# Performance work log

Hardware: AMD Instinct MI355X
Metric: run time of the kernel (lower is better)

The kernel has to match this reference:

```python
import math
import jax, jax.numpy as jnp
import numpy as np

B, S, HID = 1, 2048, 4096
NH, NKV, D = 32, 8, 128
THETA = 10000.0


def setup_inputs() -> dict:
    key = jax.random.key(0)
    k1, k2, k3, k4, k5 = jax.random.split(key, 5)
    hidden_states = jax.random.normal(k1, (B, S, HID), dtype=jnp.float32)
    k_cache = jax.random.normal(k2, (B, NKV, S, D), dtype=jnp.float32)
    v_cache = jax.random.normal(k3, (B, NKV, S, D), dtype=jnp.float32)
    Wq = jax.random.normal(k4, (HID, NH * D), dtype=jnp.float32) * 0.02
    Wo = jax.random.normal(k5, (NH * D, HID), dtype=jnp.float32) * 0.02
    position_ids = jnp.broadcast_to(jnp.arange(S, dtype=jnp.int32), (B, S))
    # causal mask: True = masked out (torch.where(mask, -10000, scores))
    attention_mask = jnp.broadcast_to(
        jnp.triu(jnp.ones((S, S), dtype=bool), k=1)[None, None], (B, 1, S, S)
    )
    return {
        "hidden_states": hidden_states,
        "k_cache": k_cache,
        "v_cache": v_cache,
        "Wq": Wq,
        "Wo": Wo,
        "position_ids": position_ids,
        "attention_mask": attention_mask,
    }


def _rotate_half(x):
    x1, x2 = jnp.split(x, 2, axis=-1)
    return jnp.concatenate([-x2, x1], axis=-1)


def _rope_tables(position_ids):
    # Llama rotary embedding gathered at position_ids -> [B, 1, S, D]
    inv_freq = 1.0 / (THETA ** (jnp.arange(0, D, 2, dtype=jnp.float32) / D))
    freqs = position_ids[..., None].astype(jnp.float32) * inv_freq  # [B, S, D/2]
    emb = jnp.concatenate([freqs, freqs], axis=-1)  # [B, S, D]
    return jnp.cos(emb)[:, None], jnp.sin(emb)[:, None]


def reference(hidden_states, k_cache, v_cache, Wq, Wo, position_ids, attention_mask):
    G = NH // NKV  # GQA group size
    # q projection: [B, S, HID] -> [B, NH, S, D]
    q = (hidden_states @ Wq).reshape(B, S, NH, D).transpose(0, 2, 1, 3)
    cos, sin = _rope_tables(position_ids)
    q = q * cos + _rotate_half(q) * sin
    # GQA without materializing repeat_kv: group query heads over kv heads
    qg = q.reshape(B, NKV, G, S, D)
    scores = jnp.einsum("bkgsd,bktd->bkgst", qg, k_cache) / math.sqrt(D)
    scores = scores.reshape(B, NH, S, S)
    scores = jnp.where(attention_mask, jnp.float32(-10000.0), scores)
    probs = jax.nn.softmax(scores.astype(jnp.float32), axis=-1).astype(q.dtype)
    out = jnp.einsum("bkgst,bktd->bkgsd", probs.reshape(B, NKV, G, S, S), v_cache)
    out = out.reshape(B, NH, S, D).transpose(0, 2, 1, 3).reshape(B, S, NH * D)
    return out @ Wo
```

## Files before the change

### kernel.cpp

```cpp
#include <hip/hip_runtime.h>
#include <cstdint>
#include <cstddef>

#define S_LEN 2048
#define HID 4096
#define NH 32
#define NKV 8
#define HD 128

typedef __attribute__((ext_vector_type(4))) float f32x4;
typedef __attribute__((ext_vector_type(8))) short bf16x8;

__device__ __forceinline__ unsigned short f2bf(float f) {
  union { float f; uint32_t u; } v; v.f = f;
  uint32_t r = v.u + 0x7FFFu + ((v.u >> 16) & 1u);
  return (unsigned short)(r >> 16);
}

__global__ void cvt_bf16_kernel(const float* __restrict__ in,
                                unsigned short* __restrict__ out, int n4) {
  int i = blockIdx.x * blockDim.x + threadIdx.x;
  if (i >= n4) return;
  float4 v = ((const float4*)in)[i];
  ushort4 o;
  o.x = f2bf(v.x); o.y = f2bf(v.y); o.z = f2bf(v.z); o.w = f2bf(v.w);
  ((ushort4*)out)[i] = o;
}

__global__ __launch_bounds__(256) void transpose_cvt2_kernel(
    const float* __restrict__ in0, unsigned short* __restrict__ out0,
    const float* __restrict__ in1, unsigned short* __restrict__ out1,
    int R, int C) {
  __shared__ float tile[64][65];
  const float* inb = (blockIdx.z == 0) ? in0 : in1;
  unsigned short* outb = (blockIdx.z == 0) ? out0 : out1;
  const int c0 = blockIdx.x * 64, r0 = blockIdx.y * 64;
  const int tid = threadIdx.x;
#pragma unroll
  for (int p = 0; p < 4; ++p) {
    const int ch = p * 256 + tid;
    const int r = ch >> 4, off = (ch & 15) << 2;
    *(float4*)&tile[r][off] = *(const float4*)(inb + (size_t)(r0 + r) * C + c0 + off);
  }
  __syncthreads();
#pragma unroll
  for (int p = 0; p < 2; ++p) {
    const int ch = p * 256 + tid;
    const int i = ch >> 3, j0 = (ch & 7) << 3;
    bf16x8 v;
#pragma unroll
    for (int k = 0; k < 8; ++k) v[k] = (short)f2bf(tile[j0 + k][i]);
    *(bf16x8*)(outb + (size_t)(c0 + i) * R + r0 + j0) = v;
  }
}

__global__ __launch_bounds__(256) void transpose_cvt_kernel(
    const float* __restrict__ in, unsigned short* __restrict__ out, int R, int C) {
  __shared__ float tile[64][65];
  const int b = blockIdx.z;
  const float* inb = in + (size_t)b * R * C;
  unsigned short* outb = out + (size_t)b * R * C;
  const int c0 = blockIdx.x * 64, r0 = blockIdx.y * 64;
  const int tid = threadIdx.x;
#pragma unroll
  for (int p = 0; p < 4; ++p) {
    const int ch = p * 256 + tid;
    const int r = ch >> 4, off = (ch & 15) << 2;
    *(float4*)&tile[r][off] = *(const float4*)(inb + (size_t)(r0 + r) * C + c0 + off);
  }
  __syncthreads();
#pragma unroll
  for (int p = 0; p < 2; ++p) {
    const int ch = p * 256 + tid;
    const int i = ch >> 3, j0 = (ch & 7) << 3;
    bf16x8 v;
#pragma unroll
    for (int k = 0; k < 8; ++k) v[k] = (short)f2bf(tile[j0 + k][i]);
    *(bf16x8*)(outb + (size_t)(c0 + i) * R + r0 + j0) = v;
  }
}

__global__ __launch_bounds__(256, 2) void gemm_bt_kernel(
    const unsigned short* __restrict__ A, const unsigned short* __restrict__ BT,
    float* __restrict__ C, int M, int N, int K) {
  __shared__ __align__(16) unsigned short As[128 * 64];
  __shared__ __align__(16) unsigned short Bs[128 * 64];
  const int tid = threadIdx.x;
  const int lane = tid & 63;
  const int wid = tid >> 6;
  const int wm = (wid >> 1) * 64, wn = (wid & 1) * 64;
  const int g = blockIdx.x;
  const int xcd = g & 7, local = g >> 3;
  const int m0 = (xcd * 2 + (local & 1)) * 128;
  const int n0 = (local >> 1) * 128;
  const int lr = lane & 15;
  const int quad = lane >> 4;
  const int sw = lr & 7;
  f32x4 acc[4][4] = {};
  for (int kt = 0; kt < K; kt += 64) {
    __syncthreads();
#pragma unroll
    for (int p = 0; p < 4; ++p) {
      const int c = p * 256 + tid;
      const int r = c >> 3, jsrc = (c & 7) ^ (r & 7);
      __builtin_amdgcn_global_load_lds(
          (const __attribute__((address_space(1))) void*)(A + (size_t)(m0 + r) * K + kt + jsrc * 8),
          (__attribute__((address_space(3))) void*)(As + c * 8), 16, 0, 0);
      __builtin_amdgcn_global_load_lds(
          (const __attribute__((address_space(1))) void*)(BT + (size_t)(n0 + r) * K + kt + jsrc * 8),
          (__attribute__((address_space(3))) void*)(Bs + c * 8), 16, 0, 0);
    }
    __syncthreads();
#pragma unroll
    for (int h = 0; h < 2; ++h) {
      const int pos = ((h * 4 + quad) ^ sw) << 3;
      bf16x8 a[4], b[4];
#pragma unroll
      for (int t = 0; t < 4; ++t) {
        a[t] = *(const bf16x8*)(As + (wm + t * 16 + lr) * 64 + pos);
        b[t] = *(const bf16x8*)(Bs + (wn + t * 16 + lr) * 64 + pos);
      }
#pragma unroll
      for (int mt = 0; mt < 4; ++mt)
#pragma unroll
        for (int nt = 0; nt < 4; ++nt)
          acc[mt][nt] = __builtin_amdgcn_mfma_f32_16x16x32_bf16(a[mt], b[nt], acc[mt][nt], 0, 0, 0);
    }
  }
  const int qd = quad << 2;
#pragma unroll
  for (int mt = 0; mt < 4; ++mt)
#pragma unroll
    for (int nt = 0; nt < 4; ++nt) {
      const int row = m0 + wm + mt * 16 + qd;
      const int col = n0 + wn + nt * 16 + lr;
#pragma unroll
      for (int r = 0; r < 4; ++r)
        C[(size_t)(row + r) * N + col] = acc[mt][nt][r];
    }
}

__global__ __launch_bounds__(256, 2) void gemm_rope_kernel(
    const unsigned short* __restrict__ A, const unsigned short* __restrict__ BT,
    const int* __restrict__ pos_ids, unsigned short* __restrict__ Qout) {
  __shared__ __align__(16) unsigned short As[128 * 64];
  __shared__ __align__(16) unsigned short Bs[128 * 64];
  const int tid = threadIdx.x;
  const int lane = tid & 63;
  const int wid = tid >> 6;
  const int wm = wid * 32;
  const int g = blockIdx.x;
  const int xcd = g & 7, local = g >> 3;
  const int m0 = (xcd * 2 + (local & 1)) * 128;
  const int n0 = (local >> 1) * 128;
  const int lr = lane & 15;
  const int quad = lane >> 4;
  const int sw = lr & 7;
  f32x4 acc[2][8] = {};
  for (int kt = 0; kt < HID; kt += 64) {
    __syncthreads();
#pragma unroll
    for (int p = 0; p < 4; ++p) {
      const int c = p * 256 + tid;
      const int r = c >> 3, jsrc = (c & 7) ^ (r & 7);
      __builtin_amdgcn_global_load_lds(
          (const __attribute__((address_space(1))) void*)(A + (size_t)(m0 + r) * HID + kt + jsrc * 8),
          (__attribute__((address_space(3))) void*)(As + c * 8), 16, 0, 0);
      __builtin_amdgcn_global_load_lds(
          (const __attribute__((address_space(1))) void*)(BT + (size_t)(n0 + r) * HID + kt + jsrc * 8),
          (__attribute__((address_space(3))) void*)(Bs + c * 8), 16, 0, 0);
    }
    __syncthreads();
#pragma unroll
    for (int h = 0; h < 2; ++h) {
      const int pos = ((h * 4 + quad) ^ sw) << 3;
      bf16x8 a[2], b[8];
#pragma unroll
      for (int t = 0; t < 2; ++t)
        a[t] = *(const bf16x8*)(As + (wm + t * 16 + lr) * 64 + pos);
#pragma unroll
      for (int t = 0; t < 8; ++t)
        b[t] = *(const bf16x8*)(Bs + (t * 16 + lr) * 64 + pos);
#pragma unroll
      for (int mt = 0; mt < 2; ++mt)
#pragma unroll
        for (int nt = 0; nt < 8; ++nt)
          acc[mt][nt] = __builtin_amdgcn_mfma_f32_16x16x32_bf16(a[mt], b[nt], acc[mt][nt], 0, 0, 0);
    }
  }
  const int qd = quad << 2;
  const int h = n0 >> 7;
#pragma unroll
  for (int mt = 0; mt < 2; ++mt)
#pragma unroll
    for (int r = 0; r < 4; ++r) {
      const int row = m0 + wm + mt * 16 + qd + r;
      const float pos = (float)pos_ids[row];
#pragma unroll
      for (int nt = 0; nt < 4; ++nt) {
        const int i = nt * 16 + lr;
        const float invf = __expf(-(float)(2 * i) * (9.2103403719761836f / 128.0f));
        float sn, cs;
        __sincosf(pos * invf, &sn, &cs);
        const float x1 = acc[mt][nt][r], x2 = acc[mt][nt + 4][r];
        Qout[((size_t)h * S_LEN + row) * HD + i]      = f2bf(x1 * cs - x2 * sn);
        Qout[((size_t)h * S_LEN + row) * HD + i + 64] = f2bf(x2 * cs + x1 * sn);
      }
    }
}

__global__ __launch_bounds__(256, 2) void attn_kernel(
    const unsigned short* __restrict__ Q, const unsigned short* __restrict__ Kc,
    const unsigned short* __restrict__ VT, unsigned short* __restrict__ Aout) {
  __shared__ __align__(16) unsigned short Ks[64 * 136];
  __shared__ __align__(16) unsigned short Vs[128 * 72];
  __shared__ __align__(16) unsigned short Ps[128 * 72];
  const int tid = threadIdx.x, lane = tid & 63, wid = tid >> 6;
  const int qh = blockIdx.x;
  const int qt = (blockIdx.y < 8) ? (15 - (int)blockIdx.y) : ((int)blockIdx.y - 8);
  const int kvh = qh >> 2;
  const int lr = lane & 15, quad = lane >> 4;
  const float scale = 0.08838834764831843f;

  bf16x8 qf[2][4];
#pragma unroll
  for (int mt = 0; mt < 2; ++mt)
#pragma unroll
    for (int kk = 0; kk < 4; ++kk)
      qf[mt][kk] = *(const bf16x8*)(Q + ((size_t)qh * S_LEN + qt * 128 + wid * 32 + mt * 16 + lr) * HD + kk * 32 + quad * 8);

  f32x4 o[2][8] = {};
  float lsum[2] = {0.f, 0.f};

  const int prow0 = (wid * 32 + lr) * 72;
  const int nkt = 2 * qt + 2;
  for (int kt2 = 0; kt2 < nkt; ++kt2) {
    bf16x8 kr[4], vr[4];
#pragma unroll
    for (int p = 0; p < 4; ++p) {
      const int c = p * 256 + tid;
      kr[p] = *(const bf16x8*)(Kc + ((size_t)kvh * S_LEN + kt2 * 64 + (c >> 4)) * HD + (c & 15) * 8);
      vr[p] = *(const bf16x8*)(VT + ((size_t)kvh * HD + (c >> 3)) * S_LEN + kt2 * 64 + (c & 7) * 8);
    }
    __syncthreads();
#pragma unroll
    for (int p = 0; p < 4; ++p) {
      const int c = p * 256 + tid;
      *(bf16x8*)(Ks + (c >> 4) * 136 + (c & 15) * 8) = kr[p];
      *(bf16x8*)(Vs + (c >> 3) * 72 + (c & 7) * 8) = vr[p];
    }
    __syncthreads();

    const bool dtile = (kt2 >= 2 * qt);
#pragma unroll
    for (int nt = 0; nt < 4; ++nt) {
      f32x4 s0 = {}, s1 = {};
#pragma unroll
      for (int kk = 0; kk < 4; ++kk) {
        bf16x8 kf = *(const bf16x8*)(Ks + (nt * 16 + lr) * 136 + kk * 32 + quad * 8);
        s0 = __builtin_amdgcn_mfma_f32_16x16x32_bf16(kf, qf[0][kk], s0, 0, 0, 0);
        s1 = __builtin_amdgcn_mfma_f32_16x16x32_bf16(kf, qf[1][kk], s1, 0, 0, 0);
      }
      const int skey0 = kt2 * 64 + nt * 16 + quad * 4;
#pragma unroll
      for (int mt = 0; mt < 2; ++mt) {
        const f32x4 s = mt ? s1 : s0;
        const int qrow = qt * 128 + wid * 32 + mt * 16 + lr;
        ushort4 pk;
        float ls = 0.f;
        float pv[4];
#pragma unroll
        for (int r = 0; r < 4; ++r) {
          float v = s[r] * scale - 16.0f;
          if (dtile && (skey0 + r) > qrow) v = -1e30f;
          pv[r] = __expf(v);
          ls += pv[r];
        }
        pk.x = f2bf(pv[0]); pk.y = f2bf(pv[1]); pk.z = f2bf(pv[2]); pk.w = f2bf(pv[3]);
        lsum[mt] += ls;
        *(ushort4*)(Ps + prow0 + mt * 16 * 72 + nt * 16 + quad * 4) = pk;
      }
    }
    bf16x8 pf[2][2];
#pragma unroll
    for (int mt = 0; mt < 2; ++mt)
#pragma unroll
      for (int kk = 0; kk < 2; ++kk)
        pf[mt][kk] = *(const bf16x8*)(Ps + prow0 + mt * 16 * 72 + kk * 32 + quad * 8);
#pragma unroll
    for (int dt = 0; dt < 8; ++dt)
#pragma unroll
      for (int kk = 0; kk < 2; ++kk) {
        bf16x8 vf = *(const bf16x8*)(Vs + (dt * 16 + lr) * 72 + kk * 32 + quad * 8);
        o[0][dt] = __builtin_amdgcn_mfma_f32_16x16x32_bf16(vf, pf[0][kk], o[0][dt], 0, 0, 0);
        o[1][dt] = __builtin_amdgcn_mfma_f32_16x16x32_bf16(vf, pf[1][kk], o[1][dt], 0, 0, 0);
      }
  }

#pragma unroll
  for (int mt = 0; mt < 2; ++mt) {
    float l = lsum[mt];
    l += __shfl_xor(l, 16);
    l += __shfl_xor(l, 32);
    const float inv = 1.0f / l;
    const int qrow = qt * 128 + wid * 32 + mt * 16 + lr;
#pragma unroll
    for (int dt = 0; dt < 8; ++dt) {
      ushort4 w;
      w.x = f2bf(o[mt][dt][0] * inv);
      w.y = f2bf(o[mt][dt][1] * inv);
      w.z = f2bf(o[mt][dt][2] * inv);
      w.w = f2bf(o[mt][dt][3] * inv);
      *(ushort4*)(Aout + (size_t)qrow * HID + qh * HD + dt * 16 + quad * 4) = w;
    }
  }
}

extern "C" void kernel_launch(void* const* d_in, const int* in_sizes, int n_in,
                              void* d_out, int out_size, void* d_ws, size_t ws_size,
                              hipStream_t stream) {
  const float* hidden  = (const float*)d_in[0];
  const float* k_cache = (const float*)d_in[1];
  const float* v_cache = (const float*)d_in[2];
  const float* Wq      = (const float*)d_in[3];
  const float* Wo      = (const float*)d_in[4];
  const int*   pos     = (const int*)d_in[5];
  float* out = (float*)d_out;

  char* ws = (char*)d_ws;
  unsigned short* hidden_bf = (unsigned short*)(ws + 0);
  unsigned short* attn_bf   = hidden_bf;
  unsigned short* WqT       = (unsigned short*)(ws + 16777216);
  unsigned short* WoT       = (unsigned short*)(ws + 50331648);
  unsigned short* k_bf      = (unsigned short*)(ws + 83886080);
  unsigned short* vT        = (unsigned short*)(ws + 88080384);
  unsigned short* q_bf      = (unsigned short*)(ws + 92274688);

  cvt_bf16_kernel<<<(S_LEN * HID / 4 + 255) / 256, 256, 0, stream>>>(hidden, hidden_bf, S_LEN * HID / 4);
  cvt_bf16_kernel<<<(NKV * S_LEN * HD / 4 + 255) / 256, 256, 0, stream>>>(k_cache, k_bf, NKV * S_LEN * HD / 4);
  transpose_cvt2_kernel<<<dim3(HID / 64, HID / 64, 2), 256, 0, stream>>>(Wq, WqT, Wo, WoT, HID, HID);
  transpose_cvt_kernel<<<dim3(HD / 64, S_LEN / 64, NKV), 256, 0, stream>>>(v_cache, vT, S_LEN, HD);

  gemm_rope_kernel<<<dim3((S_LEN / 128) * (HID / 128)), 256, 0, stream>>>(hidden_bf, WqT, pos, q_bf);
  attn_kernel<<<dim3(NH, S_LEN / 128), 256, 0, stream>>>(q_bf, k_bf, vT, attn_bf);
  gemm_bt_kernel<<<dim3((S_LEN / 128) * (HID / 128)), 256, 0, stream>>>(attn_bf, WoT, out, S_LEN, HID, HID);
}
```

Baseline: 421.4 us.

## Double-buffer attention K/V via direct global-to-LDS loads with swizzle and register P

Rewrites the attention inner loop to double-buffer K and V tiles in LDS using global_load_lds, with an XOR swizzle replacing padding to avoid bank conflicts. The probability tile no longer round-trips through shared memory; it is rearranged in registers with permlane swaps. exp2 with a folded scale, packed bf16 conversion instructions and s_setprio around MFMA blocks are also added. Together these aim to overlap loads with compute and cut LDS traffic and ALU work. The cost is more complex lane-permutation logic and reliance on gfx950-specific instructions, which could be wrong if the lane mapping is off.

```diff
diff --git a/kernel.cpp b/kernel.cpp
--- a/kernel.cpp
+++ b/kernel.cpp
@@ -15,6 +15,20 @@
   union { float f; uint32_t u; } v; v.f = f;
   uint32_t r = v.u + 0x7FFFu + ((v.u >> 16) & 1u);
   return (unsigned short)(r >> 16);
+}
+
+__device__ __forceinline__ float exp2_fast(float x) {
+#if __has_builtin(__builtin_amdgcn_exp2f)
+  return __builtin_amdgcn_exp2f(x);
+#else
+  float r; asm("v_exp_f32 %0, %1" : "=v"(r) : "v"(x)); return r;
+#endif
+}
+
+__device__ __forceinline__ unsigned int cvt_pk_bf16(float lo, float hi) {
+  unsigned int r;
+  asm("v_cvt_pk_bf16_f32 %0, %1, %2" : "=v"(r) : "v"(lo), "v"(hi));
+  return r;
 }
 
 __global__ void cvt_bf16_kernel(const float* __restrict__ in,
@@ -212,15 +226,15 @@
 __global__ __launch_bounds__(256, 2) void attn_kernel(
     const unsigned short* __restrict__ Q, const unsigned short* __restrict__ Kc,
     const unsigned short* __restrict__ VT, unsigned short* __restrict__ Aout) {
-  __shared__ __align__(16) unsigned short Ks[64 * 136];
-  __shared__ __align__(16) unsigned short Vs[128 * 72];
-  __shared__ __align__(16) unsigned short Ps[128 * 72];
+  __shared__ __align__(16) unsigned short Ks[2][64 * 128];
+  __shared__ __align__(16) unsigned short Vs[2][128 * 64];
   const int tid = threadIdx.x, lane = tid & 63, wid = tid >> 6;
   const int qh = blockIdx.x;
   const int qt = (blockIdx.y < 8) ? (15 - (int)blockIdx.y) : ((int)blockIdx.y - 8);
   const int kvh = qh >> 2;
   const int lr = lane & 15, quad = lane >> 4;
-  const float scale = 0.08838834764831843f;
+  const float SC = 0.12751619754705767f;
+  const float NB = -23.083120654223414f;
 
   bf16x8 qf[2][4];
 #pragma unroll
@@ -231,70 +245,101 @@
 
   f32x4 o[2][8] = {};
   float lsum[2] = {0.f, 0.f};
-
-  const int prow0 = (wid * 32 + lr) * 72;
   const int nkt = 2 * qt + 2;
-  for (int kt2 = 0; kt2 < nkt; ++kt2) {
-    bf16x8 kr[4], vr[4];
+  const int swz = lr & 7;
+
+  auto stage = [&](int buf, int kt2) {
 #pragma unroll
     for (int p = 0; p < 4; ++p) {
       const int c = p * 256 + tid;
-      kr[p] = *(const bf16x8*)(Kc + ((size_t)kvh * S_LEN + kt2 * 64 + (c >> 4)) * HD + (c & 15) * 8);
-      vr[p] = *(const bf16x8*)(VT + ((size_t)kvh * HD + (c >> 3)) * S_LEN + kt2 * 64 + (c & 7) * 8);
-    }
-    __syncthreads();
-#pragma unroll
-    for (int p = 0; p < 4; ++p) {
-      const int c = p * 256 + tid;
-      *(bf16x8*)(Ks + (c >> 4) * 136 + (c & 15) * 8) = kr[p];
-      *(bf16x8*)(Vs + (c >> 3) * 72 + (c & 7) * 8) = vr[p];
-    }
-    __syncthreads();
-
+      const int kr = c >> 4, kj = (c & 15) ^ (kr & 7);
+      __builtin_amdgcn_global_load_lds(
+          (const __attribute__((address_space(1))) void*)(Kc + ((size_t)kvh * S_LEN + kt2 * 64 + kr) * HD + kj * 8),
+          (__attribute__((address_space(3))) void*)(&Ks[buf][c * 8]), 16, 0, 0);
+      const int vr = c >> 3, vj = (c & 7) ^ (vr & 7);
+      __builtin_amdgcn_global_load_lds(
+          (const __attribute__((address_space(1))) void*)(VT + ((size_t)kvh * HD + vr) * S_LEN + kt2 * 64 + vj * 8),
+          (__attribute__((address_space(3))) void*)(&Vs[buf][c * 8]), 16, 0, 0);
+    }
+  };
+
+  stage(0, 0);
+  __syncthreads();
+
+  for (int kt2 = 0; kt2 < nkt; ++kt2) {
+    const int cur = kt2 & 1;
+    if (kt2 + 1 < nkt) stage(cur ^ 1, kt2 + 1);
+    const unsigned short* KsC = Ks[cur];
+    const unsigned short* VsC = Vs[cur];
     const bool dtile = (kt2 >= 2 * qt);
+
+    uint32_t Pw[2][4][2];
 #pragma unroll
     for (int nt = 0; nt < 4; ++nt) {
       f32x4 s0 = {}, s1 = {};
+      __builtin_amdgcn_s_setprio(1);
 #pragma unroll
       for (int kk = 0; kk < 4; ++kk) {
-        bf16x8 kf = *(const bf16x8*)(Ks + (nt * 16 + lr) * 136 + kk * 32 + quad * 8);
+        bf16x8 kf = *(const bf16x8*)(KsC + (nt * 16 + lr) * 128 + (((kk * 4 + quad) ^ swz) * 8));
         s0 = __builtin_amdgcn_mfma_f32_16x16x32_bf16(kf, qf[0][kk], s0, 0, 0, 0);
         s1 = __builtin_amdgcn_mfma_f32_16x16x32_bf16(kf, qf[1][kk], s1, 0, 0, 0);
       }
+      __builtin_amdgcn_s_setprio(0);
       const int skey0 = kt2 * 64 + nt * 16 + quad * 4;
 #pragma unroll
       for (int mt = 0; mt < 2; ++mt) {
         const f32x4 s = mt ? s1 : s0;
         const int qrow = qt * 128 + wid * 32 + mt * 16 + lr;
-        ushort4 pk;
+        float pv[4];
         float ls = 0.f;
-        float pv[4];
 #pragma unroll
         for (int r = 0; r < 4; ++r) {
-          float v = s[r] * scale - 16.0f;
+          float v = fmaf(s[r], SC, NB);
           if (dtile && (skey0 + r) > qrow) v = -1e30f;
-          pv[r] = __expf(v);
+          pv[r] = exp2_fast(v);
           ls += pv[r];
         }
-        pk.x = f2bf(pv[0]); pk.y = f2bf(pv[1]); pk.z = f2bf(pv[2]); pk.w = f2bf(pv[3]);
         lsum[mt] += ls;
-        *(ushort4*)(Ps + prow0 + mt * 16 * 72 + nt * 16 + quad * 4) = pk;
-      }
-    }
+        Pw[mt][nt][0] = cvt_pk_bf16(pv[0], pv[1]);
+        Pw[mt][nt][1] = cvt_pk_bf16(pv[2], pv[3]);
+      }
+    }
+
     bf16x8 pf[2][2];
 #pragma unroll
     for (int mt = 0; mt < 2; ++mt)
 #pragma unroll
-      for (int kk = 0; kk < 2; ++kk)
-        pf[mt][kk] = *(const bf16x8*)(Ps + prow0 + mt * 16 * 72 + kk * 32 + quad * 8);
+      for (int k = 0; k < 2; ++k) {
+        uint32_t w4[4];
+#pragma unroll
+        for (int w = 0; w < 2; ++w) {
+          uint32_t x = Pw[mt][2 * k][w], y = Pw[mt][2 * k + 1][w];
+          asm("v_permlane32_swap_b32 %0, %1" : "+v"(x), "+v"(y));
+          uint32_t xe = x, xo = x;
+          asm("v_permlane16_swap_b32 %0, %1" : "+v"(xe), "+v"(xo));
+          uint32_t ye = y, yo = y;
+          asm("v_permlane16_swap_b32 %0, %1" : "+v"(ye), "+v"(yo));
+          const bool qodd = (quad & 1) != 0;
+          w4[0 + w] = qodd ? ye : xe;
+          w4[2 + w] = qodd ? yo : xo;
+        }
+        union { uint32_t u[4]; bf16x8 v; } P;
+        P.u[0] = w4[0]; P.u[1] = w4[1]; P.u[2] = w4[2]; P.u[3] = w4[3];
+        pf[mt][k] = P.v;
+      }
+
+    __builtin_amdgcn_s_setprio(1);
 #pragma unroll
     for (int dt = 0; dt < 8; ++dt)
 #pragma unroll
       for (int kk = 0; kk < 2; ++kk) {
-        bf16x8 vf = *(const bf16x8*)(Vs + (dt * 16 + lr) * 72 + kk * 32 + quad * 8);
+        bf16x8 vf = *(const bf16x8*)(VsC + (dt * 16 + lr) * 64 + (((kk * 4 + quad) ^ swz) * 8));
         o[0][dt] = __builtin_amdgcn_mfma_f32_16x16x32_bf16(vf, pf[0][kk], o[0][dt], 0, 0, 0);
         o[1][dt] = __builtin_amdgcn_mfma_f32_16x16x32_bf16(vf, pf[1][kk], o[1][dt], 0, 0, 0);
       }
+    __builtin_amdgcn_s_setprio(0);
+
+    __syncthreads();
   }
 
 #pragma unroll
@@ -306,12 +351,10 @@
     const int qrow = qt * 128 + wid * 32 + mt * 16 + lr;
 #pragma unroll
     for (int dt = 0; dt < 8; ++dt) {
-      ushort4 w;
-      w.x = f2bf(o[mt][dt][0] * inv);
-      w.y = f2bf(o[mt][dt][1] * inv);
-      w.z = f2bf(o[mt][dt][2] * inv);
-      w.w = f2bf(o[mt][dt][3] * inv);
-      *(ushort4*)(Aout + (size_t)qrow * HID + qh * HD + dt * 16 + quad * 4) = w;
+      uint2 w;
+      w.x = cvt_pk_bf16(o[mt][dt][0] * inv, o[mt][dt][1] * inv);
+      w.y = cvt_pk_bf16(o[mt][dt][2] * inv, o[mt][dt][3] * inv);
+      *(uint2*)(Aout + (size_t)qrow * HID + qh * HD + dt * 16 + quad * 4) = w;
     }
   }
 }
```

Result: no change. 427.6 us (+1.5%).

## Double-buffer GEMM LDS tiles and use exp2/packed bf16 converts in attention

Applied to the files above, without the earlier changes.

Both projection GEMMs now stage the next K-tile into a second LDS buffer with global_load_lds while the current tile feeds the MFMAs. This leaves one barrier per iteration instead of two and is meant to hide global load latency. The attention softmax folds scale and offset into one FMA with log2e pre-multiplied and calls the hardware exp2. It also packs bf16 with v_cvt_pk_bf16_f32 in place of the software rounding routine. Doubling LDS to 64KB per block may limit occupancy under launch_bounds(256,2), and the async LDS writes rely on the trailing barrier for correctness.

```diff
diff --git a/kernel.cpp b/kernel.cpp
--- a/kernel.cpp
+++ b/kernel.cpp
@@ -15,6 +15,20 @@
   union { float f; uint32_t u; } v; v.f = f;
   uint32_t r = v.u + 0x7FFFu + ((v.u >> 16) & 1u);
   return (unsigned short)(r >> 16);
+}
+
+__device__ __forceinline__ float exp2_fast(float x) {
+#if __has_builtin(__builtin_amdgcn_exp2f)
+  return __builtin_amdgcn_exp2f(x);
+#else
+  float r; asm("v_exp_f32 %0, %1" : "=v"(r) : "v"(x)); return r;
+#endif
+}
+
+__device__ __forceinline__ unsigned int cvt_pk_bf16(float lo, float hi) {
+  unsigned int r;
+  asm("v_cvt_pk_bf16_f32 %0, %1, %2" : "=v"(r) : "v"(lo), "v"(hi));
+  return r;
 }
 
 __global__ void cvt_bf16_kernel(const float* __restrict__ in,
@@ -83,8 +97,8 @@
 __global__ __launch_bounds__(256, 2) void gemm_bt_kernel(
     const unsigned short* __restrict__ A, const unsigned short* __restrict__ BT,
     float* __restrict__ C, int M, int N, int K) {
-  __shared__ __align__(16) unsigned short As[128 * 64];
-  __shared__ __align__(16) unsigned short Bs[128 * 64];
+  __shared__ __align__(16) unsigned short As[2][128 * 64];
+  __shared__ __align__(16) unsigned short Bs[2][128 * 64];
   const int tid = threadIdx.x;
   const int lane = tid & 63;
   const int wid = tid >> 6;
@@ -96,29 +110,38 @@
   const int lr = lane & 15;
   const int quad = lane >> 4;
   const int sw = lr & 7;
-  f32x4 acc[4][4] = {};
-  for (int kt = 0; kt < K; kt += 64) {
-    __syncthreads();
+  const int nkt = K >> 6;
+
+  auto stage = [&](int buf, int kt) {
 #pragma unroll
     for (int p = 0; p < 4; ++p) {
       const int c = p * 256 + tid;
       const int r = c >> 3, jsrc = (c & 7) ^ (r & 7);
       __builtin_amdgcn_global_load_lds(
-          (const __attribute__((address_space(1))) void*)(A + (size_t)(m0 + r) * K + kt + jsrc * 8),
-          (__attribute__((address_space(3))) void*)(As + c * 8), 16, 0, 0);
+          (const __attribute__((address_space(1))) void*)(A + (size_t)(m0 + r) * K + kt * 64 + jsrc * 8),
+          (__attribute__((address_space(3))) void*)(&As[buf][c * 8]), 16, 0, 0);
       __builtin_amdgcn_global_load_lds(
-          (const __attribute__((address_space(1))) void*)(BT + (size_t)(n0 + r) * K + kt + jsrc * 8),
-          (__attribute__((address_space(3))) void*)(Bs + c * 8), 16, 0, 0);
-    }
-    __syncthreads();
+          (const __attribute__((address_space(1))) void*)(BT + (size_t)(n0 + r) * K + kt * 64 + jsrc * 8),
+          (__attribute__((address_space(3))) void*)(&Bs[buf][c * 8]), 16, 0, 0);
+    }
+  };
+
+  f32x4 acc[4][4] = {};
+  stage(0, 0);
+  __syncthreads();
+  int bufv = 0;
+  for (int t = 0; t < nkt; ++t) {
+    if (t + 1 < nkt) stage(bufv ^ 1, t + 1);
+    const unsigned short* as = As[bufv];
+    const unsigned short* bs = Bs[bufv];
 #pragma unroll
     for (int h = 0; h < 2; ++h) {
       const int pos = ((h * 4 + quad) ^ sw) << 3;
       bf16x8 a[4], b[4];
 #pragma unroll
-      for (int t = 0; t < 4; ++t) {
-        a[t] = *(const bf16x8*)(As + (wm + t * 16 + lr) * 64 + pos);
-        b[t] = *(const bf16x8*)(Bs + (wn + t * 16 + lr) * 64 + pos);
+      for (int tq = 0; tq < 4; ++tq) {
+        a[tq] = *(const bf16x8*)(as + (wm + tq * 16 + lr) * 64 + pos);
+        b[tq] = *(const bf16x8*)(bs + (wn + tq * 16 + lr) * 64 + pos);
       }
 #pragma unroll
       for (int mt = 0; mt < 4; ++mt)
@@ -126,6 +149,8 @@
         for (int nt = 0; nt < 4; ++nt)
           acc[mt][nt] = __builtin_amdgcn_mfma_f32_16x16x32_bf16(a[mt], b[nt], acc[mt][nt], 0, 0, 0);
     }
+    __syncthreads();
+    bufv ^= 1;
   }
   const int qd = quad << 2;
 #pragma unroll
@@ -143,8 +168,8 @@
 __global__ __launch_bounds__(256, 2) void gemm_rope_kernel(
     const unsigned short* __restrict__ A, const unsigned short* __restrict__ BT,
     const int* __restrict__ pos_ids, unsigned short* __restrict__ Qout) {
-  __shared__ __align__(16) unsigned short As[128 * 64];
-  __shared__ __align__(16) unsigned short Bs[128 * 64];
+  __shared__ __align__(16) unsigned short As[2][128 * 64];
+  __shared__ __align__(16) unsigned short Bs[2][128 * 64];
   const int tid = threadIdx.x;
   const int lane = tid & 63;
   const int wid = tid >> 6;
@@ -156,37 +181,48 @@
   const int lr = lane & 15;
   const int quad = lane >> 4;
   const int sw = lr & 7;
-  f32x4 acc[2][8] = {};
-  for (int kt = 0; kt < HID; kt += 64) {
-    __syncthreads();
+  const int nkt = HID >> 6;
+
+  auto stage = [&](int buf, int kt) {
 #pragma unroll
     for (int p = 0; p < 4; ++p) {
       const int c = p * 256 + tid;
       const int r = c >> 3, jsrc = (c & 7) ^ (r & 7);
       __builtin_amdgcn_global_load_lds(
-          (const __attribute__((address_space(1))) void*)(A + (size_t)(m0 + r) * HID + kt + jsrc * 8),
-          (__attribute__((address_space(3))) void*)(As + c * 8), 16, 0, 0);
+          (const __attribute__((address_space(1))) void*)(A + (size_t)(m0 + r) * HID + kt * 64 + jsrc * 8),
+          (__attribute__((address_space(3))) void*)(&As[buf][c * 8]), 16, 0, 0);
       __builtin_amdgcn_global_load_lds(
-          (const __attribute__((address_space(1))) void*)(BT + (size_t)(n0 + r) * HID + kt + jsrc * 8),
-          (__attribute__((address_space(3))) void*)(Bs + c * 8), 16, 0, 0);
-    }
-    __syncthreads();
+          (const __attribute__((address_space(1))) void*)(BT + (size_t)(n0 + r) * HID + kt * 64 + jsrc * 8),
+          (__attribute__((address_space(3))) void*)(&Bs[buf][c * 8]), 16, 0, 0);
+    }
+  };
+
+  f32x4 acc[2][8] = {};
+  stage(0, 0);
+  __syncthreads();
+  int bufv = 0;
+  for (int t = 0; t < nkt; ++t) {
+    if (t + 1 < nkt) stage(bufv ^ 1, t + 1);
+    const unsigned short* as = As[bufv];
+    const unsigned short* bs = Bs[bufv];
 #pragma unroll
     for (int h = 0; h < 2; ++h) {
       const int pos = ((h * 4 + quad) ^ sw) << 3;
       bf16x8 a[2], b[8];
 #pragma unroll
-      for (int t = 0; t < 2; ++t)
-        a[t] = *(const bf16x8*)(As + (wm + t * 16 + lr) * 64 + pos);
-#pragma unroll
-      for (int t = 0; t < 8; ++t)
-        b[t] = *(const bf16x8*)(Bs + (t * 16 + lr) * 64 + pos);
+      for (int tq = 0; tq < 2; ++tq)
+        a[tq] = *(const bf16x8*)(as + (wm + tq * 16 + lr) * 64 + pos);
+#pragma unroll
+      for (int tq = 0; tq < 8; ++tq)
+        b[tq] = *(const bf16x8*)(bs + (tq * 16 + lr) * 64 + pos);
 #pragma unroll
       for (int mt = 0; mt < 2; ++mt)
 #pragma unroll
         for (int nt = 0; nt < 8; ++nt)
           acc[mt][nt] = __builtin_amdgcn_mfma_f32_16x16x32_bf16(a[mt], b[nt], acc[mt][nt], 0, 0, 0);
     }
+    __syncthreads();
+    bufv ^= 1;
   }
   const int qd = quad << 2;
   const int h = n0 >> 7;
@@ -220,7 +256,8 @@
   const int qt = (blockIdx.y < 8) ? (15 - (int)blockIdx.y) : ((int)blockIdx.y - 8);
   const int kvh = qh >> 2;
   const int lr = lane & 15, quad = lane >> 4;
-  const float scale = 0.08838834764831843f;
+  const float SC = 0.12751619754705767f;
+  const float NB = -23.083120654223414f;
 
   bf16x8 qf[2][4];
 #pragma unroll
@@ -266,19 +303,20 @@
       for (int mt = 0; mt < 2; ++mt) {
         const f32x4 s = mt ? s1 : s0;
         const int qrow = qt * 128 + wid * 32 + mt * 16 + lr;
-        ushort4 pk;
+        float pv[4];
         float ls = 0.f;
-        float pv[4];
 #pragma unroll
         for (int r = 0; r < 4; ++r) {
-          float v = s[r] * scale - 16.0f;
+          float v = fmaf(s[r], SC, NB);
           if (dtile && (skey0 + r) > qrow) v = -1e30f;
-          pv[r] = __expf(v);
+          pv[r] = exp2_fast(v);
           ls += pv[r];
         }
-        pk.x = f2bf(pv[0]); pk.y = f2bf(pv[1]); pk.z = f2bf(pv[2]); pk.w = f2bf(pv[3]);
         lsum[mt] += ls;
-        *(ushort4*)(Ps + prow0 + mt * 16 * 72 + nt * 16 + quad * 4) = pk;
+        uint2 pk;
+        pk.x = cvt_pk_bf16(pv[0], pv[1]);
+        pk.y = cvt_pk_bf16(pv[2], pv[3]);
+        *(uint2*)(Ps + prow0 + mt * 16 * 72 + nt * 16 + quad * 4) = pk;
       }
     }
     bf16x8 pf[2][2];
@@ -306,12 +344,10 @@
     const int qrow = qt * 128 + wid * 32 + mt * 16 + lr;
 #pragma unroll
     for (int dt = 0; dt < 8; ++dt) {
-      ushort4 w;
-      w.x = f2bf(o[mt][dt][0] * inv);
-      w.y = f2bf(o[mt][dt][1] * inv);
-      w.z = f2bf(o[mt][dt][2] * inv);
-      w.w = f2bf(o[mt][dt][3] * inv);
-      *(ushort4*)(Aout + (size_t)qrow * HID + qh * HD + dt * 16 + quad * 4) = w;
+      uint2 w;
+      w.x = cvt_pk_bf16(o[mt][dt][0] * inv, o[mt][dt][1] * inv);
+      w.y = cvt_pk_bf16(o[mt][dt][2] * inv, o[mt][dt][3] * inv);
+      *(uint2*)(Aout + (size_t)qrow * HID + qh * HD + dt * 16 + quad * 4) = w;
     }
   }
 }
```

Result: no change. 422.0 us (+0.1%).
